# Kernel optimization log

Measured on AMD Instinct MI355X. Metric: run time of the kernel, lower is better.

## Reference

```python
import jax, jax.numpy as jnp
import numpy as np

EMBED = 1024
N, L = 8, 1024


def setup_inputs() -> dict:
    key = jax.random.key(0)
    ks = jax.random.split(key, 6)
    return {
        "values": jax.random.normal(ks[0], (N, L, EMBED), dtype=jnp.float32),
        "keys": jax.random.normal(ks[1], (N, L, EMBED), dtype=jnp.float32),
        "query": jax.random.normal(ks[2], (N, L, EMBED), dtype=jnp.float32),
        "mask": jax.random.randint(ks[3], (N, 1, L, L), 0, 2, dtype=jnp.int32),
        "W_out": jax.random.normal(ks[4], (EMBED, EMBED), dtype=jnp.float32) * (EMBED ** -0.5),
        "b_out": jax.random.normal(ks[5], (EMBED,), dtype=jnp.float32) * 0.01,
        "heads": 16,
    }


def reference(values, keys, query, mask, W_out, b_out, heads):
    n, q_len, embed = query.shape
    k_len = keys.shape[1]
    v_len = values.shape[1]
    head_dim = embed // heads
    # split heads: (N, len, H, D)
    v = values.reshape(n, v_len, heads, head_dim)
    k = keys.reshape(n, k_len, heads, head_dim)
    q = query.reshape(n, q_len, heads, head_dim)
    # raw dot-product scores (note: the original module never applies its Q/K/V linears)
    energy = jnp.einsum('nqhd,nkhd->nhqk', q, k)  # (N, H, Q, K)
    # faithful quirk: masked positions set to +1e-20 (not -inf), BEFORE scaling
    energy = jnp.where(mask == 0, jnp.float32(1e-20), energy)
    # faithful quirk: scale by sqrt(embed_size), not sqrt(head_dim)
    attention = jax.nn.softmax(energy / jnp.sqrt(jnp.float32(embed)), axis=3)
    out = jnp.einsum('nhqk,nkhd->nqhd', attention, v).reshape(n, q_len, embed)
    # fc_out: torch Linear stores weight (out, in); y = x @ W^T + b
    return out @ W_out.T + b_out
```

## Files before the change

### kernel.cpp

```cpp
#include <hip/hip_runtime.h>

typedef __attribute__((ext_vector_type(8))) short bf16x8;
typedef __attribute__((ext_vector_type(4))) float f32x4;
typedef unsigned short ushort_t;

#define SWZ(row, byteofs) (((row)*128) + ((byteofs) ^ (((row)&7)<<4)))

__device__ __forceinline__ unsigned short f2bf(float x){
  unsigned u = __builtin_bit_cast(unsigned, x);
  u = (u + 0x7fffu + ((u >> 16) & 1u)) >> 16;
  return (unsigned short)u;
}

__device__ __forceinline__ void gld16(const void* g, void* l){
  __builtin_amdgcn_global_load_lds((const __attribute__((address_space(1))) void*)g,
                                   (__attribute__((address_space(3))) void*)l, 16, 0, 0);
}

__global__ __launch_bounds__(256) void mask_bits_kernel(const int* __restrict__ mask,
                                                        unsigned* __restrict__ bits){
  int t = blockIdx.x * 256 + threadIdx.x;
  int u = t >> 6;
  int lane = t & 63;
  int row = u >> 4;
  int chunk = u & 15;
  int m = mask[(size_t)row * 1024 + chunk * 64 + lane];
  unsigned long long b = __ballot(m != 0);
  if (lane == 0){
    unsigned* p = bits + row * 32 + chunk * 2;
    p[0] = (unsigned)(b & 0xffffffffull);
    p[1] = (unsigned)(b >> 32);
  }
}

__global__ __launch_bounds__(256) void wconv_kernel(const float* __restrict__ W,
                                                    unsigned short* __restrict__ Wb){
  int i = blockIdx.x * 256 + threadIdx.x;
  float4 f = reinterpret_cast<const float4*>(W)[i];
  ushort4 o;
  o.x = f2bf(f.x); o.y = f2bf(f.y); o.z = f2bf(f.z); o.w = f2bf(f.w);
  reinterpret_cast<ushort4*>(Wb)[i] = o;
}

__global__ __launch_bounds__(256) void permqk_kernel(const float* __restrict__ src,
                                                     unsigned short* __restrict__ dst){
  int w = blockIdx.x * 4 + (threadIdx.x >> 6);
  int lane = threadIdx.x & 63;
  int n = w >> 11, h = (w >> 7) & 15, l8 = w & 127;
  int l = l8 * 8 + (lane >> 3);
  int dch = (lane & 7) * 8;
  const float* sp = src + ((size_t)n * 1024 + l) * 1024 + h * 64 + dch;
  float4 a = *reinterpret_cast<const float4*>(sp);
  float4 b = *reinterpret_cast<const float4*>(sp + 4);
  bf16x8 v;
  v[0]=(short)f2bf(a.x); v[1]=(short)f2bf(a.y); v[2]=(short)f2bf(a.z); v[3]=(short)f2bf(a.w);
  v[4]=(short)f2bf(b.x); v[5]=(short)f2bf(b.y); v[6]=(short)f2bf(b.z); v[7]=(short)f2bf(b.w);
  *reinterpret_cast<bf16x8*>(dst + (((size_t)n * 16 + h) * 1024 + l) * 64 + dch) = v;
}

__global__ __launch_bounds__(256) void permv_kernel(const float* __restrict__ src,
                                                    unsigned short* __restrict__ dst){
  __shared__ __attribute__((aligned(16))) unsigned short T[64*64];
  int bid = blockIdx.x;
  int n = bid >> 8, h = (bid >> 4) & 15, l0 = (bid & 15) * 64;
  int t = threadIdx.x;
  {
    int l = t >> 2, dseg = t & 3;
    const float* sp = src + ((size_t)n * 1024 + l0 + l) * 1024 + h * 64 + dseg * 16;
    float4 f0 = *reinterpret_cast<const float4*>(sp + 0);
    float4 f1 = *reinterpret_cast<const float4*>(sp + 4);
    float4 f2 = *reinterpret_cast<const float4*>(sp + 8);
    float4 f3 = *reinterpret_cast<const float4*>(sp + 12);
    bf16x8 lo, hi;
    lo[0]=(short)f2bf(f0.x); lo[1]=(short)f2bf(f0.y); lo[2]=(short)f2bf(f0.z); lo[3]=(short)f2bf(f0.w);
    lo[4]=(short)f2bf(f1.x); lo[5]=(short)f2bf(f1.y); lo[6]=(short)f2bf(f1.z); lo[7]=(short)f2bf(f1.w);
    hi[0]=(short)f2bf(f2.x); hi[1]=(short)f2bf(f2.y); hi[2]=(short)f2bf(f2.z); hi[3]=(short)f2bf(f2.w);
    hi[4]=(short)f2bf(f3.x); hi[5]=(short)f2bf(f3.y); hi[6]=(short)f2bf(f3.z); hi[7]=(short)f2bf(f3.w);
    *reinterpret_cast<bf16x8*>((char*)T + SWZ(l, dseg*32))      = lo;
    *reinterpret_cast<bf16x8*>((char*)T + SWZ(l, dseg*32 + 16)) = hi;
  }
  __syncthreads();
  {
    int d = t >> 2, lseg = t & 3;
    for (int j = 0; j < 2; ++j){
      bf16x8 wv;
      #pragma unroll
      for (int i = 0; i < 8; ++i){
        int l = lseg*16 + j*8 + i;
        wv[i] = *(const short*)((const char*)T + (size_t)l*128 + ((d*2) ^ (i<<4)));
      }
      *reinterpret_cast<bf16x8*>(dst + (((size_t)n * 16 + h) * 64 + d) * 1024 + l0 + lseg*16 + j*8) = wv;
    }
  }
}

__global__ __launch_bounds__(256) void attn_kernel(
    const unsigned short* __restrict__ Qb, const unsigned short* __restrict__ Kb,
    const unsigned short* __restrict__ Vtg, const unsigned* __restrict__ bits,
    unsigned short* __restrict__ Obf)
{
  __shared__ __attribute__((aligned(16))) unsigned short Kt[2][64*64];
  __shared__ __attribute__((aligned(16))) unsigned short Vt[2][64*64];
  __shared__ __attribute__((aligned(16))) unsigned short Pl[4][16*64];

  int bid = blockIdx.x;
  int wg = ((bid & 7) << 8) | (bid >> 3);
  int qb = wg & 15, h = (wg >> 4) & 15, n = wg >> 8;

  int tid = threadIdx.x, wid = tid >> 6, lane = tid & 63, lg = lane >> 4, lc = lane & 15;
  int qbase = qb * 64 + wid * 16;

  const unsigned short* Kh = Kb  + ((size_t)(n*16 + h)) * 1024 * 64;
  const unsigned short* Vh = Vtg + ((size_t)(n*16 + h)) * 64 * 1024;
  const unsigned short* Qh = Qb  + ((size_t)(n*16 + h)) * 1024 * 64;

  bf16x8 qf[2];
  qf[0] = *reinterpret_cast<const bf16x8*>(Qh + (size_t)(qbase + lc) * 64 + lg*8);
  qf[1] = *reinterpret_cast<const bf16x8*>(Qh + (size_t)(qbase + lc) * 64 + lg*8 + 32);

  const int s0 = tid, s1 = tid + 256;
  const int r0 = s0 >> 3, c0 = ((s0 & 7) * 16) ^ ((r0 & 7) << 4);
  const int r1 = s1 >> 3, c1 = ((s1 & 7) * 16) ^ ((r1 & 7) << 4);

#define STAGE(KB, BUF) do { \
    gld16((const char*)Kh + ((size_t)((KB)*64 + r0) * 128 + c0), (char*)Kt[BUF] + s0*16); \
    gld16((const char*)Kh + ((size_t)((KB)*64 + r1) * 128 + c1), (char*)Kt[BUF] + s1*16); \
    gld16((const char*)Vh + ((size_t)r0 * 2048 + (KB)*128 + c0), (char*)Vt[BUF] + s0*16); \
    gld16((const char*)Vh + ((size_t)r1 * 2048 + (KB)*128 + c1), (char*)Vt[BUF] + s1*16); \
  } while(0)

  f32x4 acc[4];
  for (int i = 0; i < 4; ++i) acc[i] = (f32x4){0.f,0.f,0.f,0.f};
  float lsum[4] = {0.f,0.f,0.f,0.f};
  const float scale = 0.03125f;

  STAGE(0, 0);
  int cur = 0;

  for (int kb = 0; kb < 16; ++kb){
    __syncthreads();
    if (kb < 15) STAGE(kb + 1, cur ^ 1);

    unsigned words[4][2];
    {
      const unsigned* bp = bits + (size_t)(n*1024 + qbase + lg*4) * 32 + kb*2;
      #pragma unroll
      for (int r = 0; r < 4; ++r){ words[r][0] = bp[r*32]; words[r][1] = bp[r*32 + 1]; }
    }

    f32x4 S[4];
    #pragma unroll
    for (int t = 0; t < 4; ++t) S[t] = (f32x4){0.f,0.f,0.f,0.f};
    __builtin_amdgcn_s_setprio(1);
    #pragma unroll
    for (int t = 0; t < 4; ++t)
      #pragma unroll
      for (int c = 0; c < 2; ++c){
        bf16x8 kf = *reinterpret_cast<const bf16x8*>((const char*)Kt[cur] + SWZ(t*16 + lc, lg*16 + c*64));
        S[t] = __builtin_amdgcn_mfma_f32_16x16x32_bf16(qf[c], kf, S[t], 0, 0, 0);
      }
    __builtin_amdgcn_s_setprio(0);

    float p[4][4];
    #pragma unroll
    for (int t = 0; t < 4; ++t){
      int bitidx = ((t & 1) << 4) + lc;
      #pragma unroll
      for (int r = 0; r < 4; ++r){
        bool mk = (words[r][t>>1] >> bitidx) & 1u;
        p[t][r] = mk ? __expf(S[t][r] * scale) : 1.0f;
      }
    }
    #pragma unroll
    for (int r = 0; r < 4; ++r)
      lsum[r] += (p[0][r] + p[1][r]) + (p[2][r] + p[3][r]);

    unsigned short* pl = &Pl[wid][0];
    #pragma unroll
    for (int t = 0; t < 4; ++t)
      #pragma unroll
      for (int r = 0; r < 4; ++r)
        *(unsigned short*)((char*)pl + SWZ(lg*4 + r, (t*16 + lc)*2)) = f2bf(p[t][r]);

    __builtin_amdgcn_s_setprio(1);
    #pragma unroll
    for (int kc = 0; kc < 2; ++kc){
      bf16x8 af = *reinterpret_cast<const bf16x8*>((const char*)pl + SWZ(lc, lg*16 + kc*64));
      #pragma unroll
      for (int t2 = 0; t2 < 4; ++t2){
        bf16x8 vf = *reinterpret_cast<const bf16x8*>((const char*)Vt[cur] + SWZ(t2*16 + lc, lg*16 + kc*64));
        acc[t2] = __builtin_amdgcn_mfma_f32_16x16x32_bf16(af, vf, acc[t2], 0, 0, 0);
      }
    }
    __builtin_amdgcn_s_setprio(0);
    cur ^= 1;
  }
#undef STAGE

  #pragma unroll
  for (int r = 0; r < 4; ++r){
    float s = lsum[r];
    for (int d = 1; d < 16; d <<= 1) s += __shfl_xor(s, d, 64);
    float inv = 1.0f / s;
    size_t qg = (size_t)(n*1024 + qbase + lg*4 + r);
    unsigned short* op = Obf + (qg * 16 + h) * 64;
    #pragma unroll
    for (int t2 = 0; t2 < 4; ++t2)
      op[t2*16 + lc] = f2bf(acc[t2][r] * inv);
  }
}

__global__ __launch_bounds__(256) void out_gemm_kernel(
    const unsigned short* __restrict__ A, const unsigned short* __restrict__ B,
    const float* __restrict__ bias, float* __restrict__ out)
{
  __shared__ __attribute__((aligned(16))) unsigned short As[128*64];
  __shared__ __attribute__((aligned(16))) unsigned short Bs[128*64];

  int mb = blockIdx.x;
  int nb = blockIdx.y;
  int tid = threadIdx.x, wid = tid >> 6, lane = tid & 63, lg = lane >> 4, lc = lane & 15;
  int wr = wid >> 1, wc = wid & 1;

  f32x4 acc[4][4];
  for (int m = 0; m < 4; ++m)
    for (int nn2 = 0; nn2 < 4; ++nn2) acc[m][nn2] = (f32x4){0.f,0.f,0.f,0.f};

  for (int kb = 0; kb < 16; ++kb){
    __syncthreads();
    {
      int row = tid >> 1;
      int half = tid & 1;
      const unsigned short* ap = A + (size_t)(mb*128 + row) * 1024 + kb*64 + half*32;
      const unsigned short* bp = B + (size_t)(nb*128 + row) * 1024 + kb*64 + half*32;
      for (int j = 0; j < 4; ++j){
        *reinterpret_cast<bf16x8*>((char*)As + SWZ(row, half*64 + j*16)) = *reinterpret_cast<const bf16x8*>(ap + j*8);
        *reinterpret_cast<bf16x8*>((char*)Bs + SWZ(row, half*64 + j*16)) = *reinterpret_cast<const bf16x8*>(bp + j*8);
      }
    }
    __syncthreads();
    for (int kc = 0; kc < 2; ++kc){
      bf16x8 af[4], bfr[4];
      for (int m = 0; m < 4; ++m)
        af[m] = *reinterpret_cast<const bf16x8*>((const char*)As + SWZ(wr*64 + m*16 + lc, kc*64 + lg*16));
      for (int nn2 = 0; nn2 < 4; ++nn2)
        bfr[nn2] = *reinterpret_cast<const bf16x8*>((const char*)Bs + SWZ(wc*64 + nn2*16 + lc, kc*64 + lg*16));
      __builtin_amdgcn_s_setprio(1);
      for (int m = 0; m < 4; ++m)
        for (int nn2 = 0; nn2 < 4; ++nn2)
          acc[m][nn2] = __builtin_amdgcn_mfma_f32_16x16x32_bf16(af[m], bfr[nn2], acc[m][nn2], 0, 0, 0);
      __builtin_amdgcn_s_setprio(0);
    }
  }

  for (int nn2 = 0; nn2 < 4; ++nn2){
    int col = nb*128 + wc*64 + nn2*16 + lc;
    float bv = bias[col];
    for (int m = 0; m < 4; ++m){
      int rowb = mb*128 + wr*64 + m*16 + lg*4;
      for (int r = 0; r < 4; ++r)
        out[(size_t)(rowb + r) * 1024 + col] = acc[m][nn2][r] + bv;
    }
  }
}

extern "C" void kernel_launch(void* const* d_in, const int* in_sizes, int n_in,
                              void* d_out, int out_size, void* d_ws, size_t ws_size,
                              hipStream_t stream) {
  const float* V  = (const float*)d_in[0];
  const float* K  = (const float*)d_in[1];
  const float* Q  = (const float*)d_in[2];
  const int* mask = (const int*)d_in[3];
  const float* W  = (const float*)d_in[4];
  const float* b  = (const float*)d_in[5];
  float* out = (float*)d_out;

  char* ws = (char*)d_ws;
  unsigned* bits       = (unsigned*)ws;
  unsigned short* Wb   = (unsigned short*)(ws + (1u<<20));
  unsigned short* Obf  = (unsigned short*)(ws + (3u<<20));
  unsigned short* Vtg  = (unsigned short*)(ws + (19u<<20));
  unsigned short* Qb   = (unsigned short*)d_out;
  unsigned short* Kb   = Qb + (size_t)8*1024*1024;

  mask_bits_kernel<<<32768, 256, 0, stream>>>(mask, bits);
  wconv_kernel<<<1024, 256, 0, stream>>>(W, Wb);
  permqk_kernel<<<4096, 256, 0, stream>>>(Q, Qb);
  permqk_kernel<<<4096, 256, 0, stream>>>(K, Kb);
  permv_kernel<<<2048, 256, 0, stream>>>(V, Vtg);
  attn_kernel<<<2048, 256, 0, stream>>>(Qb, Kb, Vtg, bits, Obf);
  dim3 g(64, 8);
  out_gemm_kernel<<<g, 256, 0, stream>>>(Obf, Wb, b, out);
}
```

Baseline: 149.0 us.

## Load Q directly in attention, double-buffer output GEMM, use packed bf16 conversion

Removes the separate Q permute/convert kernel; the attention kernel now reads fp32 Q straight from the input and converts it to bf16 in registers. This saves one full pass over Q in global memory and one launch. The output GEMM switches from synchronous register-staged tile loads to double-buffered direct global-to-LDS loads, so the next tile's transfer overlaps the current tile's MFMAs, at the cost of doubled shared memory. All bf16 conversions now use the packed HIP intrinsic instead of manual per-element bit rounding.

```diff
diff --git a/kernel.cpp b/kernel.cpp
--- a/kernel.cpp
+++ b/kernel.cpp
@@ -1,21 +1,23 @@
 #include <hip/hip_runtime.h>
+#include <hip/hip_bf16.h>
 
 typedef __attribute__((ext_vector_type(8))) short bf16x8;
 typedef __attribute__((ext_vector_type(4))) float f32x4;
-typedef unsigned short ushort_t;
 
 #define SWZ(row, byteofs) (((row)*128) + ((byteofs) ^ (((row)&7)<<4)))
 
-__device__ __forceinline__ unsigned short f2bf(float x){
-  unsigned u = __builtin_bit_cast(unsigned, x);
-  u = (u + 0x7fffu + ((u >> 16) & 1u)) >> 16;
-  return (unsigned short)u;
+__device__ __forceinline__ unsigned pk2(float a, float b){
+  __hip_bfloat162 h = __float22bfloat162_rn(make_float2(a, b));
+  unsigned u; __builtin_memcpy(&u, &h, 4);
+  return u;
 }
 
 __device__ __forceinline__ void gld16(const void* g, void* l){
   __builtin_amdgcn_global_load_lds((const __attribute__((address_space(1))) void*)g,
                                    (__attribute__((address_space(3))) void*)l, 16, 0, 0);
 }
+
+union bfpack { bf16x8 v; unsigned u[4]; uint4 q; };
 
 __global__ __launch_bounds__(256) void mask_bits_kernel(const int* __restrict__ mask,
                                                         unsigned* __restrict__ bits){
@@ -37,9 +39,8 @@
                                                     unsigned short* __restrict__ Wb){
   int i = blockIdx.x * 256 + threadIdx.x;
   float4 f = reinterpret_cast<const float4*>(W)[i];
-  ushort4 o;
-  o.x = f2bf(f.x); o.y = f2bf(f.y); o.z = f2bf(f.z); o.w = f2bf(f.w);
-  reinterpret_cast<ushort4*>(Wb)[i] = o;
+  uint2 o = make_uint2(pk2(f.x, f.y), pk2(f.z, f.w));
+  reinterpret_cast<uint2*>(Wb)[i] = o;
 }
 
 __global__ __launch_bounds__(256) void permqk_kernel(const float* __restrict__ src,
@@ -52,10 +53,8 @@
   const float* sp = src + ((size_t)n * 1024 + l) * 1024 + h * 64 + dch;
   float4 a = *reinterpret_cast<const float4*>(sp);
   float4 b = *reinterpret_cast<const float4*>(sp + 4);
-  bf16x8 v;
-  v[0]=(short)f2bf(a.x); v[1]=(short)f2bf(a.y); v[2]=(short)f2bf(a.z); v[3]=(short)f2bf(a.w);
-  v[4]=(short)f2bf(b.x); v[5]=(short)f2bf(b.y); v[6]=(short)f2bf(b.z); v[7]=(short)f2bf(b.w);
-  *reinterpret_cast<bf16x8*>(dst + (((size_t)n * 16 + h) * 1024 + l) * 64 + dch) = v;
+  uint4 o = make_uint4(pk2(a.x,a.y), pk2(a.z,a.w), pk2(b.x,b.y), pk2(b.z,b.w));
+  *reinterpret_cast<uint4*>(dst + (((size_t)n * 16 + h) * 1024 + l) * 64 + dch) = o;
 }
 
 __global__ __launch_bounds__(256) void permv_kernel(const float* __restrict__ src,
@@ -71,13 +70,10 @@
     float4 f1 = *reinterpret_cast<const float4*>(sp + 4);
     float4 f2 = *reinterpret_cast<const float4*>(sp + 8);
     float4 f3 = *reinterpret_cast<const float4*>(sp + 12);
-    bf16x8 lo, hi;
-    lo[0]=(short)f2bf(f0.x); lo[1]=(short)f2bf(f0.y); lo[2]=(short)f2bf(f0.z); lo[3]=(short)f2bf(f0.w);
-    lo[4]=(short)f2bf(f1.x); lo[5]=(short)f2bf(f1.y); lo[6]=(short)f2bf(f1.z); lo[7]=(short)f2bf(f1.w);
-    hi[0]=(short)f2bf(f2.x); hi[1]=(short)f2bf(f2.y); hi[2]=(short)f2bf(f2.z); hi[3]=(short)f2bf(f2.w);
-    hi[4]=(short)f2bf(f3.x); hi[5]=(short)f2bf(f3.y); hi[6]=(short)f2bf(f3.z); hi[7]=(short)f2bf(f3.w);
-    *reinterpret_cast<bf16x8*>((char*)T + SWZ(l, dseg*32))      = lo;
-    *reinterpret_cast<bf16x8*>((char*)T + SWZ(l, dseg*32 + 16)) = hi;
+    uint4 lo = make_uint4(pk2(f0.x,f0.y), pk2(f0.z,f0.w), pk2(f1.x,f1.y), pk2(f1.z,f1.w));
+    uint4 hi = make_uint4(pk2(f2.x,f2.y), pk2(f2.z,f2.w), pk2(f3.x,f3.y), pk2(f3.z,f3.w));
+    *reinterpret_cast<uint4*>((char*)T + SWZ(l, dseg*32))      = lo;
+    *reinterpret_cast<uint4*>((char*)T + SWZ(l, dseg*32 + 16)) = hi;
   }
   __syncthreads();
   {
@@ -95,7 +91,7 @@
 }
 
 __global__ __launch_bounds__(256) void attn_kernel(
-    const unsigned short* __restrict__ Qb, const unsigned short* __restrict__ Kb,
+    const float* __restrict__ Q, const unsigned short* __restrict__ Kb,
     const unsigned short* __restrict__ Vtg, const unsigned* __restrict__ bits,
     unsigned short* __restrict__ Obf)
 {
@@ -112,11 +108,20 @@
 
   const unsigned short* Kh = Kb  + ((size_t)(n*16 + h)) * 1024 * 64;
   const unsigned short* Vh = Vtg + ((size_t)(n*16 + h)) * 64 * 1024;
-  const unsigned short* Qh = Qb  + ((size_t)(n*16 + h)) * 1024 * 64;
 
   bf16x8 qf[2];
-  qf[0] = *reinterpret_cast<const bf16x8*>(Qh + (size_t)(qbase + lc) * 64 + lg*8);
-  qf[1] = *reinterpret_cast<const bf16x8*>(Qh + (size_t)(qbase + lc) * 64 + lg*8 + 32);
+  {
+    const float* qp = Q + (size_t)(n*1024 + qbase + lc) * 1024 + h*64;
+    #pragma unroll
+    for (int c = 0; c < 2; ++c){
+      float4 a0 = *reinterpret_cast<const float4*>(qp + c*32 + lg*8);
+      float4 a1 = *reinterpret_cast<const float4*>(qp + c*32 + lg*8 + 4);
+      bfpack pk;
+      pk.u[0] = pk2(a0.x,a0.y); pk.u[1] = pk2(a0.z,a0.w);
+      pk.u[2] = pk2(a1.x,a1.y); pk.u[3] = pk2(a1.z,a1.w);
+      qf[c] = pk.v;
+    }
+  }
 
   const int s0 = tid, s1 = tid + 256;
   const int r0 = s0 >> 3, c0 = ((s0 & 7) * 16) ^ ((r0 & 7) << 4);
@@ -177,10 +182,15 @@
 
     unsigned short* pl = &Pl[wid][0];
     #pragma unroll
-    for (int t = 0; t < 4; ++t)
-      #pragma unroll
-      for (int r = 0; r < 4; ++r)
-        *(unsigned short*)((char*)pl + SWZ(lg*4 + r, (t*16 + lc)*2)) = f2bf(p[t][r]);
+    for (int t = 0; t < 4; ++t){
+      unsigned w01 = pk2(p[t][0], p[t][1]);
+      unsigned w23 = pk2(p[t][2], p[t][3]);
+      int colb = (t*16 + lc)*2;
+      *(unsigned short*)((char*)pl + SWZ(lg*4 + 0, colb)) = (unsigned short)w01;
+      *(unsigned short*)((char*)pl + SWZ(lg*4 + 1, colb)) = (unsigned short)(w01 >> 16);
+      *(unsigned short*)((char*)pl + SWZ(lg*4 + 2, colb)) = (unsigned short)w23;
+      *(unsigned short*)((char*)pl + SWZ(lg*4 + 3, colb)) = (unsigned short)(w23 >> 16);
+    }
 
     __builtin_amdgcn_s_setprio(1);
     #pragma unroll
@@ -204,9 +214,12 @@
     float inv = 1.0f / s;
     size_t qg = (size_t)(n*1024 + qbase + lg*4 + r);
     unsigned short* op = Obf + (qg * 16 + h) * 64;
-    #pragma unroll
-    for (int t2 = 0; t2 < 4; ++t2)
-      op[t2*16 + lc] = f2bf(acc[t2][r] * inv);
+    unsigned w01 = pk2(acc[0][r]*inv, acc[1][r]*inv);
+    unsigned w23 = pk2(acc[2][r]*inv, acc[3][r]*inv);
+    op[0*16 + lc] = (unsigned short)w01;
+    op[1*16 + lc] = (unsigned short)(w01 >> 16);
+    op[2*16 + lc] = (unsigned short)w23;
+    op[3*16 + lc] = (unsigned short)(w23 >> 16);
   }
 }
 
@@ -214,44 +227,61 @@
     const unsigned short* __restrict__ A, const unsigned short* __restrict__ B,
     const float* __restrict__ bias, float* __restrict__ out)
 {
-  __shared__ __attribute__((aligned(16))) unsigned short As[128*64];
-  __shared__ __attribute__((aligned(16))) unsigned short Bs[128*64];
+  __shared__ __attribute__((aligned(16))) unsigned short As[2][128*64];
+  __shared__ __attribute__((aligned(16))) unsigned short Bs[2][128*64];
 
   int mb = blockIdx.x;
   int nb = blockIdx.y;
   int tid = threadIdx.x, wid = tid >> 6, lane = tid & 63, lg = lane >> 4, lc = lane & 15;
   int wr = wid >> 1, wc = wid & 1;
 
+  int rr[4], cc[4];
+  #pragma unroll
+  for (int i = 0; i < 4; ++i){
+    int s = tid + 256*i;
+    rr[i] = s >> 3;
+    cc[i] = ((s & 7) * 16) ^ ((rr[i] & 7) << 4);
+  }
+
+#define GSTAGE(KB, BUF) do { \
+    _Pragma("unroll") \
+    for (int i = 0; i < 4; ++i){ \
+      int s = tid + 256*i; \
+      gld16((const char*)A + ((size_t)(mb*128 + rr[i]) * 1024 + (KB)*64) * 2 + cc[i], (char*)As[BUF] + s*16); \
+      gld16((const char*)B + ((size_t)(nb*128 + rr[i]) * 1024 + (KB)*64) * 2 + cc[i], (char*)Bs[BUF] + s*16); \
+    } \
+  } while(0)
+
   f32x4 acc[4][4];
   for (int m = 0; m < 4; ++m)
     for (int nn2 = 0; nn2 < 4; ++nn2) acc[m][nn2] = (f32x4){0.f,0.f,0.f,0.f};
 
+  GSTAGE(0, 0);
+  int cur = 0;
+
   for (int kb = 0; kb < 16; ++kb){
     __syncthreads();
-    {
-      int row = tid >> 1;
-      int half = tid & 1;
-      const unsigned short* ap = A + (size_t)(mb*128 + row) * 1024 + kb*64 + half*32;
-      const unsigned short* bp = B + (size_t)(nb*128 + row) * 1024 + kb*64 + half*32;
-      for (int j = 0; j < 4; ++j){
-        *reinterpret_cast<bf16x8*>((char*)As + SWZ(row, half*64 + j*16)) = *reinterpret_cast<const bf16x8*>(ap + j*8);
-        *reinterpret_cast<bf16x8*>((char*)Bs + SWZ(row, half*64 + j*16)) = *reinterpret_cast<const bf16x8*>(bp + j*8);
-      }
-    }
-    __syncthreads();
+    if (kb < 15) GSTAGE(kb + 1, cur ^ 1);
+    #pragma unroll
     for (int kc = 0; kc < 2; ++kc){
       bf16x8 af[4], bfr[4];
+      #pragma unroll
       for (int m = 0; m < 4; ++m)
-        af[m] = *reinterpret_cast<const bf16x8*>((const char*)As + SWZ(wr*64 + m*16 + lc, kc*64 + lg*16));
+        af[m] = *reinterpret_cast<const bf16x8*>((const char*)As[cur] + SWZ(wr*64 + m*16 + lc, kc*64 + lg*16));
+      #pragma unroll
       for (int nn2 = 0; nn2 < 4; ++nn2)
-        bfr[nn2] = *reinterpret_cast<const bf16x8*>((const char*)Bs + SWZ(wc*64 + nn2*16 + lc, kc*64 + lg*16));
+        bfr[nn2] = *reinterpret_cast<const bf16x8*>((const char*)Bs[cur] + SWZ(wc*64 + nn2*16 + lc, kc*64 + lg*16));
       __builtin_amdgcn_s_setprio(1);
+      #pragma unroll
       for (int m = 0; m < 4; ++m)
+        #pragma unroll
         for (int nn2 = 0; nn2 < 4; ++nn2)
           acc[m][nn2] = __builtin_amdgcn_mfma_f32_16x16x32_bf16(af[m], bfr[nn2], acc[m][nn2], 0, 0, 0);
       __builtin_amdgcn_s_setprio(0);
     }
-  }
+    cur ^= 1;
+  }
+#undef GSTAGE
 
   for (int nn2 = 0; nn2 < 4; ++nn2){
     int col = nb*128 + wc*64 + nn2*16 + lc;
@@ -280,15 +310,13 @@
   unsigned short* Wb   = (unsigned short*)(ws + (1u<<20));
   unsigned short* Obf  = (unsigned short*)(ws + (3u<<20));
   unsigned short* Vtg  = (unsigned short*)(ws + (19u<<20));
-  unsigned short* Qb   = (unsigned short*)d_out;
-  unsigned short* Kb   = Qb + (size_t)8*1024*1024;
+  unsigned short* Kb   = (unsigned short*)d_out;
 
   mask_bits_kernel<<<32768, 256, 0, stream>>>(mask, bits);
   wconv_kernel<<<1024, 256, 0, stream>>>(W, Wb);
-  permqk_kernel<<<4096, 256, 0, stream>>>(Q, Qb);
   permqk_kernel<<<4096, 256, 0, stream>>>(K, Kb);
   permv_kernel<<<2048, 256, 0, stream>>>(V, Vtg);
-  attn_kernel<<<2048, 256, 0, stream>>>(Qb, Kb, Vtg, bits, Obf);
+  attn_kernel<<<2048, 256, 0, stream>>>(Q, Kb, Vtg, bits, Obf);
   dim3 g(64, 8);
   out_gemm_kernel<<<g, 256, 0, stream>>>(Obf, Wb, b, out);
 }
```

Measured after the change: 135.1 us. -9.3%, faster.
